# Performance work log

Hardware: AMD Instinct MI355X
Metric: run time of the kernel (lower is better)

## Reference

```python
import jax, jax.numpy as jnp
import numpy as np

DIM = 1024
HIDDEN = 4096
NNZ = 262144
X_SHAPE = (2, 256, DIM)


def setup_inputs() -> dict:
    key = jax.random.key(0)
    ks = jax.random.split(key, 13)
    return {
        "x": jax.random.normal(ks[0], X_SHAPE, dtype=jnp.float32),
        "up_row": jax.random.randint(ks[1], (NNZ,), 0, HIDDEN),
        "up_col": jax.random.randint(ks[2], (NNZ,), 0, DIM),
        "up_val": jax.random.normal(ks[3], (NNZ,), dtype=jnp.float32),
        "up_bias": jax.random.normal(ks[4], (HIDDEN,), dtype=jnp.float32),
        "gate_row": jax.random.randint(ks[5], (NNZ,), 0, HIDDEN),
        "gate_col": jax.random.randint(ks[6], (NNZ,), 0, DIM),
        "gate_val": jax.random.normal(ks[7], (NNZ,), dtype=jnp.float32),
        "gate_bias": jax.random.normal(ks[8], (HIDDEN,), dtype=jnp.float32),
        "down_row": jax.random.randint(ks[9], (NNZ,), 0, DIM),
        "down_col": jax.random.randint(ks[10], (NNZ,), 0, HIDDEN),
        "down_val": jax.random.normal(ks[11], (NNZ,), dtype=jnp.float32),
        "down_bias": jax.random.normal(ks[12], (DIM,), dtype=jnp.float32),
    }


def _sparse_linear(x2d, row, col, val, bias, out_features):
    # x2d: [T, in_features]; COO: row -> out_features, col -> in_features
    weighted = x2d[:, col] * val  # [T, nnz], same expanded form as torch gather*mul
    # scatter_add over rows == segment_sum over the nnz axis
    out = jax.ops.segment_sum(weighted.T, row, num_segments=out_features).T  # [T, out]
    return out + bias


def reference(x, up_row, up_col, up_val, up_bias,
              gate_row, gate_col, gate_val, gate_bias,
              down_row, down_col, down_val, down_bias):
    in_shape = x.shape
    x2d = x.reshape(-1, DIM)  # [T, dim]
    up = _sparse_linear(x2d, up_row, up_col, up_val, up_bias, HIDDEN)
    gate = _sparse_linear(x2d, gate_row, gate_col, gate_val, gate_bias, HIDDEN)
    hidden = jax.nn.silu(up) * gate  # [T, hidden]
    down = _sparse_linear(hidden, down_row, down_col, down_val, down_bias, DIM)
    return (x2d + down).reshape(in_shape)
```

## Files before the change

### kernel.cpp

```cpp
#include <hip/hip_runtime.h>
#include <hip/hip_bf16.h>
#include <stdint.h>


#define DIM_    1024
#define HIDDEN_ 4096
#define NNZ_    262144
#define TTOK_   512
#define PAD_    24

typedef __attribute__((ext_vector_type(8))) short short8;
typedef __attribute__((ext_vector_type(4))) float float4v;

__device__ inline unsigned short f2bf(float f) {
    union { float f; unsigned int u; } c; c.f = f;
    unsigned int u = c.u;
    unsigned int r = u + 0x7fffu + ((u >> 16) & 1u);
    return (unsigned short)(r >> 16);
}

__device__ inline void async16(const unsigned short* g, unsigned short* l) {
    __builtin_amdgcn_global_load_lds(
        (const __attribute__((address_space(1))) unsigned int*)g,
        (__attribute__((address_space(3))) unsigned int*)l, 16, 0, 0);
}

#define XC_ ((TTOK_ * DIM_) / 4)

__global__ void prep_kernel(const float* __restrict__ x,
                            const float* __restrict__ down_bias,
                            unsigned short* __restrict__ xb,
                            float* __restrict__ out) {
    unsigned int id = blockIdx.x * blockDim.x + threadIdx.x;
    if (id < XC_) {
        float4 v = ((const float4*)x)[id];
        ushort4 o;
        o.x = f2bf(v.x); o.y = f2bf(v.y); o.z = f2bf(v.z); o.w = f2bf(v.w);
        ((ushort4*)xb)[id] = o;
    } else {
        unsigned int i = id - XC_;
        float4 v = ((const float4*)x)[i];
        int d = (i * 4) & (DIM_ - 1);
        const float4 b = *(const float4*)(down_bias + d);
        float4 o;
        o.x = v.x + b.x; o.y = v.y + b.y; o.z = v.z + b.z; o.w = v.w + b.w;
        ((float4*)out)[i] = o;
    }
}

__global__ __launch_bounds__(256) void bin_kernel(
    const int* __restrict__ ur, const int* __restrict__ uc, const float* __restrict__ uv,
    const int* __restrict__ gr, const int* __restrict__ gc, const float* __restrict__ gv,
    const int* __restrict__ dr, const int* __restrict__ dc, const float* __restrict__ dv,
    uint2* __restrict__ bands, int* __restrict__ cnt) {
    __shared__ int lcount[256];
    const int b = blockIdx.x;
    const int t = threadIdx.x;
    const int mat = b >> 8;
    const int chunk = b & 255;
    const int*   rs = (mat == 0) ? ur : (mat == 1) ? gr : dr;
    const int*   cs = (mat == 0) ? uc : (mat == 1) ? gc : dc;
    const float* vs = (mat == 0) ? uv : (mat == 1) ? gv : dv;
    const int shift = (mat == 2) ? 2 : 4;
    const int rmask = (mat == 2) ? 3 : 15;
    lcount[t] = 0;
    __syncthreads();

    const int base = chunk * 1024 + t * 4;
    int4   r4 = *(const int4*)(rs + base);
    int4   c4 = *(const int4*)(cs + base);
    float4 v4 = *(const float4*)(vs + base);
    uint2* mbase = bands + mat * (256 * 256 * PAD_);
    int   rr[4] = {r4.x, r4.y, r4.z, r4.w};
    int   cc[4] = {c4.x, c4.y, c4.z, c4.w};
    float vv[4] = {v4.x, v4.y, v4.z, v4.w};
    #pragma unroll
    for (int j = 0; j < 4; ++j) {
        const int band = rr[j] >> shift;
        const int pos = atomicAdd(&lcount[band], 1);
        if (pos < PAD_) {
            uint2 e;
            e.x = ((unsigned int)(rr[j] & rmask) << 12) | (unsigned int)cc[j];
            e.y = __float_as_uint(vv[j]);
            mbase[(band * 256 + chunk) * PAD_ + pos] = e;
        }
    }
    __syncthreads();
    cnt[(mat * 256 + t) * 256 + chunk] = lcount[t];
}

__global__ __launch_bounds__(512) void build_kernel(
    const uint2* __restrict__ bands,
    const int* __restrict__ cnt,
    unsigned short* __restrict__ WUP,
    unsigned short* __restrict__ WGATE,
    unsigned short* __restrict__ WDOWN) {
    __shared__ float acc[16 * 1024];
    __shared__ int lcnt[256];
    const int b = blockIdx.x;
    const int t = threadIdx.x;
    const int mat = b >> 8;
    const int band = b & 255;
    unsigned int width;
    unsigned short* out;
    if (mat == 0)      { width = 1024; out = WUP + band * 16 * 1024; }
    else if (mat == 1) { width = 1024; out = WGATE + band * 16 * 1024; }
    else               { width = 4096; out = WDOWN + band * 4 * 4096; }

    for (int k = 0; k < 8; ++k)
        *(float4*)&acc[(k * 512 + t) * 4] = make_float4(0.f, 0.f, 0.f, 0.f);
    if (t < 256) lcnt[t] = cnt[(mat * 256 + band) * 256 + t];
    __syncthreads();

    const int chunk = t & 255;
    const int half = t >> 8;
    const uint2* seg = bands + (((mat * 256 + band) * 256) + chunk) * PAD_;
    const int c = lcnt[chunk];

    if (half == 0) {
        uint4 q[6];
        const uint4* sp = (const uint4*)seg;
        #pragma unroll
        for (int i = 0; i < 6; ++i) q[i] = sp[i];
        #pragma unroll
        for (int j = 0; j < 12; ++j) {
            const unsigned int ex = (j & 1) ? q[j >> 1].z : q[j >> 1].x;
            const unsigned int ey = (j & 1) ? q[j >> 1].w : q[j >> 1].y;
            if (j < c)
                atomicAdd(&acc[(ex >> 12) * width + (ex & 0xFFFu)],
                          __uint_as_float(ey));
        }
    } else {
        for (int j = 12; j < c && j < PAD_; ++j) {
            uint2 e = seg[j];
            atomicAdd(&acc[(e.x >> 12) * width + (e.x & 0xFFFu)],
                      __uint_as_float(e.y));
        }
    }
    __syncthreads();

    for (int k = 0; k < 8; ++k) {
        const int cc = (k * 512 + t) * 4;
        ushort4 o;
        o.x = f2bf(acc[cc]);     o.y = f2bf(acc[cc + 1]);
        o.z = f2bf(acc[cc + 2]); o.w = f2bf(acc[cc + 3]);
        *(ushort4*)(out + cc) = o;
    }
}

__global__ __launch_bounds__(256) void gemm_upgate_kernel(
    const unsigned short* __restrict__ xb,
    const unsigned short* __restrict__ wup,
    const unsigned short* __restrict__ wgate,
    const float* __restrict__ up_bias,
    const float* __restrict__ gate_bias,
    unsigned short* __restrict__ hid) {
    __shared__ unsigned short sA[64 * 32];
    __shared__ unsigned short sB[128 * 32];
    const int t = threadIdx.x;
    const int m0 = blockIdx.y * 64;
    const int n0 = blockIdx.x * 128;
    const int w = t >> 6, l = t & 63;
    const int wm = (w >> 1) * 32, wn = (w & 1) * 64;
    const int lr = l & 15, lkq = (l >> 4);

    float4v acc[2][2][4];
    for (int p = 0; p < 2; ++p)
        for (int im = 0; im < 2; ++im)
            for (int in = 0; in < 4; ++in)
                acc[p][im][in] = float4v{0.f, 0.f, 0.f, 0.f};

    const int srow = t >> 2, scol = (t & 3) * 8;

    for (int p = 0; p < 2; ++p) {
        const unsigned short* W = p ? wgate : wup;
        for (int k0 = 0; k0 < DIM_; k0 += 32) {
            async16(xb + (m0 + srow) * DIM_ + k0 + scol, &sA[t * 8]);
            async16(W + (n0 + srow) * DIM_ + k0 + scol, &sB[t * 8]);
            async16(W + (n0 + 64 + srow) * DIM_ + k0 + scol, &sB[(t + 256) * 8]);
            __syncthreads();
            short8 a[2], b[4];
            for (int im = 0; im < 2; ++im)
                a[im] = *(const short8*)&sA[(wm + im * 16 + lr) * 32 + lkq * 8];
            for (int in = 0; in < 4; ++in)
                b[in] = *(const short8*)&sB[(wn + in * 16 + lr) * 32 + lkq * 8];
            for (int im = 0; im < 2; ++im)
                for (int in = 0; in < 4; ++in)
                    acc[p][im][in] = __builtin_amdgcn_mfma_f32_16x16x32_bf16(
                        a[im], b[in], acc[p][im][in], 0, 0, 0);
            __syncthreads();
        }
    }

    for (int im = 0; im < 2; ++im) {
        for (int in = 0; in < 4; ++in) {
            const int n = n0 + wn + in * 16 + lr;
            const float ub = up_bias[n], gb = gate_bias[n];
            for (int r = 0; r < 4; ++r) {
                const int m = m0 + wm + im * 16 + lkq * 4 + r;
                const float u = acc[0][im][in][r] + ub;
                const float g = acc[1][im][in][r] + gb;
                const float h = (u / (1.f + __expf(-u))) * g;
                hid[m * HIDDEN_ + n] = f2bf(h);
            }
        }
    }
}

__global__ __launch_bounds__(256) void gemm_down_kernel(
    const unsigned short* __restrict__ hid,
    const unsigned short* __restrict__ wdown,
    float* __restrict__ out) {
    __shared__ unsigned short sA[64 * 32];
    __shared__ unsigned short sB[64 * 32];
    const int t = threadIdx.x;
    const int n0 = blockIdx.x * 64;
    const int m0 = blockIdx.y * 64;
    const int kb = blockIdx.z * 1024;
    const int w = t >> 6, l = t & 63;
    const int wm = (w >> 1) * 32, wn = (w & 1) * 32;
    const int lr = l & 15, lkq = (l >> 4);

    float4v acc[2][2];
    for (int im = 0; im < 2; ++im)
        for (int in = 0; in < 2; ++in)
            acc[im][in] = float4v{0.f, 0.f, 0.f, 0.f};

    const int srow = t >> 2, scol = (t & 3) * 8;

    for (int k0 = kb; k0 < kb + 1024; k0 += 32) {
        async16(hid + (m0 + srow) * HIDDEN_ + k0 + scol, &sA[t * 8]);
        async16(wdown + (n0 + srow) * HIDDEN_ + k0 + scol, &sB[t * 8]);
        __syncthreads();
        short8 a[2], b[2];
        for (int im = 0; im < 2; ++im)
            a[im] = *(const short8*)&sA[(wm + im * 16 + lr) * 32 + lkq * 8];
        for (int in = 0; in < 2; ++in)
            b[in] = *(const short8*)&sB[(wn + in * 16 + lr) * 32 + lkq * 8];
        for (int im = 0; im < 2; ++im)
            for (int in = 0; in < 2; ++in)
                acc[im][in] = __builtin_amdgcn_mfma_f32_16x16x32_bf16(
                    a[im], b[in], acc[im][in], 0, 0, 0);
        __syncthreads();
    }

    for (int im = 0; im < 2; ++im) {
        for (int in = 0; in < 2; ++in) {
            const int n = n0 + wn + in * 16 + lr;
            for (int r = 0; r < 4; ++r) {
                const int m = m0 + wm + im * 16 + lkq * 4 + r;
                atomicAdd(out + m * DIM_ + n, acc[im][in][r]);
            }
        }
    }
}

extern "C" void kernel_launch(void* const* d_in, const int* in_sizes, int n_in,
                              void* d_out, int out_size, void* d_ws, size_t ws_size,
                              hipStream_t stream) {
    const float* x         = (const float*)d_in[0];
    const int*   up_row    = (const int*)d_in[1];
    const int*   up_col    = (const int*)d_in[2];
    const float* up_val    = (const float*)d_in[3];
    const float* up_bias   = (const float*)d_in[4];
    const int*   gate_row  = (const int*)d_in[5];
    const int*   gate_col  = (const int*)d_in[6];
    const float* gate_val  = (const float*)d_in[7];
    const float* gate_bias = (const float*)d_in[8];
    const int*   down_row  = (const int*)d_in[9];
    const int*   down_col  = (const int*)d_in[10];
    const float* down_val  = (const float*)d_in[11];
    const float* down_bias = (const float*)d_in[12];
    float* out = (float*)d_out;

    unsigned char* ws = (unsigned char*)d_ws;
    unsigned short* WUP   = (unsigned short*)(ws);
    unsigned short* WGATE = (unsigned short*)(ws + (8u << 20));
    unsigned short* WDOWN = (unsigned short*)(ws + (16u << 20));
    unsigned short* XB    = (unsigned short*)(ws + (24u << 20));
    unsigned short* HID   = (unsigned short*)(ws + (25u << 20));
    uint2*          BANDS = (uint2*)(ws + (29u << 20));
    int*            CNT   = (int*)(ws + (66u << 20));

    prep_kernel<<<1024, 256, 0, stream>>>(x, down_bias, XB, out);

    bin_kernel<<<768, 256, 0, stream>>>(
        up_row, up_col, up_val, gate_row, gate_col, gate_val,
        down_row, down_col, down_val, BANDS, CNT);

    build_kernel<<<768, 512, 0, stream>>>(BANDS, CNT, WUP, WGATE, WDOWN);

    gemm_upgate_kernel<<<dim3(HIDDEN_ / 128, TTOK_ / 64), 256, 0, stream>>>(
        XB, WUP, WGATE, up_bias, gate_bias, HID);

    gemm_down_kernel<<<dim3(DIM_ / 64, TTOK_ / 64, 4), 256, 0, stream>>>(
        HID, WDOWN, out);
}
```

Before: 154.2 us.

## Merge prep into bin kernel and interleave up/gate GEMM with smaller N tile

```diff
diff --git a/kernel.cpp b/kernel.cpp
--- a/kernel.cpp
+++ b/kernel.cpp
@@ -27,35 +27,38 @@
 
 #define XC_ ((TTOK_ * DIM_) / 4)
 
-__global__ void prep_kernel(const float* __restrict__ x,
-                            const float* __restrict__ down_bias,
-                            unsigned short* __restrict__ xb,
-                            float* __restrict__ out) {
-    unsigned int id = blockIdx.x * blockDim.x + threadIdx.x;
-    if (id < XC_) {
-        float4 v = ((const float4*)x)[id];
-        ushort4 o;
-        o.x = f2bf(v.x); o.y = f2bf(v.y); o.z = f2bf(v.z); o.w = f2bf(v.w);
-        ((ushort4*)xb)[id] = o;
-    } else {
-        unsigned int i = id - XC_;
-        float4 v = ((const float4*)x)[i];
-        int d = (i * 4) & (DIM_ - 1);
-        const float4 b = *(const float4*)(down_bias + d);
-        float4 o;
-        o.x = v.x + b.x; o.y = v.y + b.y; o.z = v.z + b.z; o.w = v.w + b.w;
-        ((float4*)out)[i] = o;
-    }
-}
-
-__global__ __launch_bounds__(256) void bin_kernel(
+__global__ __launch_bounds__(256) void bin_prep_kernel(
     const int* __restrict__ ur, const int* __restrict__ uc, const float* __restrict__ uv,
     const int* __restrict__ gr, const int* __restrict__ gc, const float* __restrict__ gv,
     const int* __restrict__ dr, const int* __restrict__ dc, const float* __restrict__ dv,
-    uint2* __restrict__ bands, int* __restrict__ cnt) {
-    __shared__ int lcount[256];
+    const float* __restrict__ x, const float* __restrict__ down_bias,
+    uint2* __restrict__ bands, int* __restrict__ cnt,
+    unsigned short* __restrict__ xb, float* __restrict__ out) {
     const int b = blockIdx.x;
     const int t = threadIdx.x;
+    if (b >= 768) {
+        const unsigned int u0 = (b - 768) * 1024 + t * 4;
+        #pragma unroll
+        for (int q = 0; q < 4; ++q) {
+            const unsigned int id = u0 + q;
+            if (id < XC_) {
+                float4 v = ((const float4*)x)[id];
+                ushort4 o;
+                o.x = f2bf(v.x); o.y = f2bf(v.y); o.z = f2bf(v.z); o.w = f2bf(v.w);
+                ((ushort4*)xb)[id] = o;
+            } else {
+                const unsigned int i = id - XC_;
+                float4 v = ((const float4*)x)[i];
+                const int d = (i * 4) & (DIM_ - 1);
+                const float4 bb = *(const float4*)(down_bias + d);
+                float4 o;
+                o.x = v.x + bb.x; o.y = v.y + bb.y; o.z = v.z + bb.z; o.w = v.w + bb.w;
+                ((float4*)out)[i] = o;
+            }
+        }
+        return;
+    }
+    __shared__ int lcount[256];
     const int mat = b >> 8;
     const int chunk = b & 255;
     const int*   rs = (mat == 0) ? ur : (mat == 1) ? gr : dr;
@@ -156,50 +159,54 @@
     const float* __restrict__ gate_bias,
     unsigned short* __restrict__ hid) {
     __shared__ unsigned short sA[64 * 32];
-    __shared__ unsigned short sB[128 * 32];
+    __shared__ unsigned short sBu[64 * 32];
+    __shared__ unsigned short sBg[64 * 32];
     const int t = threadIdx.x;
+    const int n0 = blockIdx.x * 64;
     const int m0 = blockIdx.y * 64;
-    const int n0 = blockIdx.x * 128;
     const int w = t >> 6, l = t & 63;
-    const int wm = (w >> 1) * 32, wn = (w & 1) * 64;
+    const int wm = (w >> 1) * 32, wn = (w & 1) * 32;
     const int lr = l & 15, lkq = (l >> 4);
 
-    float4v acc[2][2][4];
-    for (int p = 0; p < 2; ++p)
+    float4v au[2][2], ag[2][2];
+    for (int im = 0; im < 2; ++im)
+        for (int in = 0; in < 2; ++in) {
+            au[im][in] = float4v{0.f, 0.f, 0.f, 0.f};
+            ag[im][in] = float4v{0.f, 0.f, 0.f, 0.f};
+        }
+
+    const int srow = t >> 2, scol = (t & 3) * 8;
+
+    for (int k0 = 0; k0 < DIM_; k0 += 32) {
+        async16(xb + (m0 + srow) * DIM_ + k0 + scol, &sA[t * 8]);
+        async16(wup + (n0 + srow) * DIM_ + k0 + scol, &sBu[t * 8]);
+        async16(wgate + (n0 + srow) * DIM_ + k0 + scol, &sBg[t * 8]);
+        __syncthreads();
+        short8 a[2], bu[2], bg[2];
         for (int im = 0; im < 2; ++im)
-            for (int in = 0; in < 4; ++in)
-                acc[p][im][in] = float4v{0.f, 0.f, 0.f, 0.f};
-
-    const int srow = t >> 2, scol = (t & 3) * 8;
-
-    for (int p = 0; p < 2; ++p) {
-        const unsigned short* W = p ? wgate : wup;
-        for (int k0 = 0; k0 < DIM_; k0 += 32) {
-            async16(xb + (m0 + srow) * DIM_ + k0 + scol, &sA[t * 8]);
-            async16(W + (n0 + srow) * DIM_ + k0 + scol, &sB[t * 8]);
-            async16(W + (n0 + 64 + srow) * DIM_ + k0 + scol, &sB[(t + 256) * 8]);
-            __syncthreads();
-            short8 a[2], b[4];
-            for (int im = 0; im < 2; ++im)
-                a[im] = *(const short8*)&sA[(wm + im * 16 + lr) * 32 + lkq * 8];
-            for (int in = 0; in < 4; ++in)
-                b[in] = *(const short8*)&sB[(wn + in * 16 + lr) * 32 + lkq * 8];
-            for (int im = 0; im < 2; ++im)
-                for (int in = 0; in < 4; ++in)
-                    acc[p][im][in] = __builtin_amdgcn_mfma_f32_16x16x32_bf16(
-                        a[im], b[in], acc[p][im][in], 0, 0, 0);
-            __syncthreads();
-        }
+            a[im] = *(const short8*)&sA[(wm + im * 16 + lr) * 32 + lkq * 8];
+        for (int in = 0; in < 2; ++in) {
+            bu[in] = *(const short8*)&sBu[(wn + in * 16 + lr) * 32 + lkq * 8];
+            bg[in] = *(const short8*)&sBg[(wn + in * 16 + lr) * 32 + lkq * 8];
+        }
+        for (int im = 0; im < 2; ++im)
+            for (int in = 0; in < 2; ++in) {
+                au[im][in] = __builtin_amdgcn_mfma_f32_16x16x32_bf16(
+                    a[im], bu[in], au[im][in], 0, 0, 0);
+                ag[im][in] = __builtin_amdgcn_mfma_f32_16x16x32_bf16(
+                    a[im], bg[in], ag[im][in], 0, 0, 0);
+            }
+        __syncthreads();
     }
 
     for (int im = 0; im < 2; ++im) {
-        for (int in = 0; in < 4; ++in) {
+        for (int in = 0; in < 2; ++in) {
             const int n = n0 + wn + in * 16 + lr;
             const float ub = up_bias[n], gb = gate_bias[n];
             for (int r = 0; r < 4; ++r) {
                 const int m = m0 + wm + im * 16 + lkq * 4 + r;
-                const float u = acc[0][im][in][r] + ub;
-                const float g = acc[1][im][in][r] + gb;
+                const float u = au[im][in][r] + ub;
+                const float g = ag[im][in][r] + gb;
                 const float h = (u / (1.f + __expf(-u))) * g;
                 hid[m * HIDDEN_ + n] = f2bf(h);
             }
@@ -282,15 +289,13 @@
     uint2*          BANDS = (uint2*)(ws + (29u << 20));
     int*            CNT   = (int*)(ws + (66u << 20));
 
-    prep_kernel<<<1024, 256, 0, stream>>>(x, down_bias, XB, out);
-
-    bin_kernel<<<768, 256, 0, stream>>>(
+    bin_prep_kernel<<<1024, 256, 0, stream>>>(
         up_row, up_col, up_val, gate_row, gate_col, gate_val,
-        down_row, down_col, down_val, BANDS, CNT);
+        down_row, down_col, down_val, x, down_bias, BANDS, CNT, XB, out);
 
     build_kernel<<<768, 512, 0, stream>>>(BANDS, CNT, WUP, WGATE, WDOWN);
 
-    gemm_upgate_kernel<<<dim3(HIDDEN_ / 128, TTOK_ / 64), 256, 0, stream>>>(
+    gemm_upgate_kernel<<<dim3(HIDDEN_ / 64, TTOK_ / 64), 256, 0, stream>>>(
         XB, WUP, WGATE, up_bias, gate_bias, HID);
 
     gemm_down_kernel<<<dim3(DIM_ / 64, TTOK_ / 64, 4), 256, 0, stream>>>(
```

New measurement: 140.2 us. 9.1% less time.
